# Optimization experiments

Measured on AMD Instinct MI355X. Metric: run time of the kernel, lower is better.

The kernel has to match this reference:

```python
import jax, jax.numpy as jnp
import numpy as np
import math

B, L, D, H, DFF, NL = 32, 512, 768, 12, 3072, 2
E = D // H
VOCAB = 30522
TOPK = int(1 * math.log(L))   # factor=1 -> 6
MA = 25                        # series_decomp moving-average kernel (Autoformer default)
CMID = D // 2                  # 384 conv channels
PLEN = (L - 2) // 2            # 255 pooled length
LATENT, NCELLS = 32, 2034


def _ln(x, g, b, eps=1e-5):
    mu = x.mean(-1, keepdims=True)
    v = ((x - mu) ** 2).mean(-1, keepdims=True)
    return (x - mu) * jax.lax.rsqrt(v + eps) * g + b


def _decomp(x):
    # series_decomp: x - moving_avg(x, k=25) with replicate padding, via cumsum
    pad = (MA - 1) // 2
    xp = jnp.concatenate([jnp.repeat(x[:, :1], pad, 1), x, jnp.repeat(x[:, -1:], pad, 1)], 1)
    cs = jnp.cumsum(xp, axis=1)
    cs = jnp.concatenate([jnp.zeros_like(cs[:, :1]), cs], 1)
    mm = (cs[:, MA:] - cs[:, :-MA]) / MA  # [B,L,D]
    return x - mm


def _autocorr(q, k, v):
    # q,k,v: [B,L,H,E] -> FFT autocorrelation + top-k delay aggregation (inference path)
    qt = jnp.transpose(q, (0, 2, 3, 1))
    kt = jnp.transpose(k, (0, 2, 3, 1))
    vt = jnp.transpose(v, (0, 2, 3, 1))  # [B,H,E,L]
    corr = jnp.fft.irfft(jnp.fft.rfft(qt, axis=-1) * jnp.conj(jnp.fft.rfft(kt, axis=-1)), n=L, axis=-1)
    mean_value = corr.mean(axis=(1, 2))                      # [B,L]
    weights, delay = jax.lax.top_k(mean_value, TOPK)         # [B,K]
    w = jax.nn.softmax(weights, axis=-1)                     # [B,K]
    tv = jnp.concatenate([vt, vt], -1)                       # [B,H,E,2L]
    idx = jnp.arange(L)[None, None, :] + delay[:, :, None]   # [B,K,L]
    pat = jnp.take_along_axis(tv[:, None], idx[:, :, None, None, :], axis=-1)  # [B,K,H,E,L]
    V = jnp.einsum('bkhel,bk->bhel', pat, w)
    return jnp.transpose(V, (0, 3, 1, 2))                    # [B,L,H,E]


def _forward(input_ids, word_emb, pos_emb, tok_emb, emb_ln_g, emb_ln_b,
             Wq, bq, Wk, bk, Wv, bv, Wo, bo, Wc1, bc1, Wc2, bc2,
             norm_g, norm_b, conv_w, conv_b, bn_g, bn_b, bn_m, bn_v,
             lin1_w, lin1_b, ln2_g, ln2_b, lin2_w, lin2_b):
    # BertEmbeddings (token_type all zeros)
    x = word_emb[input_ids] + pos_emb[None, :L] + tok_emb[0][None, None]
    x = _ln(x, emb_ln_g, emb_ln_b, 1e-12)
    # Autoformer encoder layers
    for l in range(NL):
        q = (x @ Wq[l].T + bq[l]).reshape(B, L, H, E)
        k = (x @ Wk[l].T + bk[l]).reshape(B, L, H, E)
        v = (x @ Wv[l].T + bv[l]).reshape(B, L, H, E)
        a = _autocorr(q, k, v).reshape(B, L, D) @ Wo[l].T + bo[l]
        x = _decomp(x + a)
        y = jax.nn.gelu(x @ Wc1[l].T + bc1[l], approximate=False) @ Wc2[l].T + bc2[l]
        x = _decomp(x + y)
    # my_Layernorm
    x_hat = _ln(x, norm_g, norm_b)
    att_out = x_hat - x_hat.mean(axis=1, keepdims=True)      # [B,L,D]
    # Prediction head
    z = jnp.transpose(att_out, (0, 2, 1))                    # [B,D,L]
    c = jax.lax.conv_general_dilated(z, conv_w, (1,), 'VALID',
                                     dimension_numbers=('NCH', 'OIH', 'NCH')) + conv_b[None, :, None]
    c = (c - bn_m[None, :, None]) * jax.lax.rsqrt(bn_v + 1e-5)[None, :, None] * bn_g[None, :, None] + bn_b[None, :, None]
    c = jax.nn.elu(c)                                        # [B,384,510]
    p = c.reshape(B, CMID, PLEN, 2).max(-1)                  # maxpool k=2
    f = p.reshape(B, CMID * PLEN)
    h = jax.nn.elu(_ln(f @ lin1_w.T + lin1_b, ln2_g, ln2_b))
    return jax.nn.sigmoid(h @ lin2_w.T + lin2_b)             # [B,2034]


def setup_inputs() -> dict:
    key = jax.random.key(0)
    ks = iter(jax.random.split(key, 64))
    n = lambda *s: 0.02 * jax.random.normal(next(ks), s, dtype=jnp.float32)
    return dict(
        input_ids=jax.random.randint(next(ks), (B, L), 0, VOCAB),
        word_emb=n(VOCAB, D), pos_emb=n(L, D), tok_emb=n(2, D),
        emb_ln_g=jnp.ones((D,), jnp.float32), emb_ln_b=jnp.zeros((D,), jnp.float32),
        Wq=n(NL, D, D), bq=n(NL, D), Wk=n(NL, D, D), bk=n(NL, D),
        Wv=n(NL, D, D), bv=n(NL, D), Wo=n(NL, D, D), bo=n(NL, D),
        Wc1=n(NL, DFF, D), bc1=n(NL, DFF), Wc2=n(NL, D, DFF), bc2=n(NL, D),
        norm_g=jnp.ones((D,), jnp.float32), norm_b=jnp.zeros((D,), jnp.float32),
        conv_w=n(CMID, D, 3), conv_b=n(CMID),
        bn_g=jnp.ones((CMID,), jnp.float32), bn_b=jnp.zeros((CMID,), jnp.float32),
        bn_m=n(CMID), bn_v=jax.random.uniform(next(ks), (CMID,), jnp.float32) + 0.5,
        lin1_w=n(LATENT, CMID * PLEN), lin1_b=n(LATENT),
        ln2_g=jnp.ones((LATENT,), jnp.float32), ln2_b=jnp.zeros((LATENT,), jnp.float32),
        lin2_w=n(NCELLS, LATENT), lin2_b=n(NCELLS),
    )


def reference(input_ids, word_emb, pos_emb, tok_emb, emb_ln_g, emb_ln_b,
              Wq, bq, Wk, bk, Wv, bv, Wo, bo, Wc1, bc1, Wc2, bc2,
              norm_g, norm_b, conv_w, conv_b, bn_g, bn_b, bn_m, bn_v,
              lin1_w, lin1_b, ln2_g, ln2_b, lin2_w, lin2_b):
    return _forward(input_ids, word_emb, pos_emb, tok_emb, emb_ln_g, emb_ln_b,
                    Wq, bq, Wk, bk, Wv, bv, Wo, bo, Wc1, bc1, Wc2, bc2,
                    norm_g, norm_b, conv_w, conv_b, bn_g, bn_b, bn_m, bn_v,
                    lin1_w, lin1_b, ln2_g, ln2_b, lin2_w, lin2_b)
```

## Files before the change

kernel.cpp:

```cpp
#include <hip/hip_runtime.h>
#include <hip/hip_bf16.h>

#define B_ 32
#define L_ 512
#define D_ 768
#define DFF_ 3072
#define NL_ 2
#define TOPK_ 6
#define CMID_ 384
#define CLEN_ 510
#define PLEN_ 255
#define LATENT_ 32
#define NCELLS_ 2034
#define NROWS_ (B_*L_)
#define ND_ ((size_t)B_*L_*D_)

typedef unsigned short ushort_t;
typedef __attribute__((ext_vector_type(8))) short short8;
typedef __attribute__((ext_vector_type(4))) float f32x4;

typedef const __attribute__((address_space(1))) unsigned int* gp1;
typedef __attribute__((address_space(3))) unsigned int* lp3;

static __device__ __forceinline__ void gload16(const ushort_t* g, ushort_t* l) {
  __builtin_amdgcn_global_load_lds((gp1)g, (lp3)l, 16, 0, 0);
}

static __device__ __forceinline__ float geluf(float x) {
  return 0.5f * x * (1.f + erff(x * 0.70710678118654752440f));
}
static __device__ __forceinline__ float eluf(float x) {
  return x > 0.f ? x : expm1f(x);
}
static __device__ __forceinline__ ushort_t bf16rn(float f) {
  unsigned u = __builtin_bit_cast(unsigned, f);
  u = u + 0x7FFFu + ((u >> 16) & 1u);
  return (ushort_t)(u >> 16);
}
static __device__ __forceinline__ float bf16tof(ushort_t s) {
  unsigned u = ((unsigned)s) << 16;
  return __builtin_bit_cast(float, u);
}
static __device__ __forceinline__ f32x4 mfma16(short8 a, short8 b, f32x4 c) {
  return __builtin_amdgcn_mfma_f32_16x16x32_bf16(a, b, c, 0, 0, 0);
}

__global__ void wsplit(const float* __restrict__ w, ushort_t* __restrict__ hi,
                       ushort_t* __restrict__ lo, size_t n) {
  size_t stride = (size_t)gridDim.x * blockDim.x;
  for (size_t i = (size_t)blockIdx.x * blockDim.x + threadIdx.x; i < n; i += stride) {
    float v = w[i];
    ushort_t h = bf16rn(v);
    hi[i] = h;
    if (lo) lo[i] = bf16rn(v - bf16tof(h));
  }
}

__global__ __launch_bounds__(256) void tsplit(const float* __restrict__ in, ushort_t* __restrict__ hiT,
                                              ushort_t* __restrict__ loT) {
  __shared__ float tile[32][33];
  size_t off = (size_t)blockIdx.z * D_ * D_;
  int bx = blockIdx.x * 32, by = blockIdx.y * 32;
  int tx = threadIdx.x & 31, ty = threadIdx.x >> 5;
#pragma unroll
  for (int i = 0; i < 32; i += 8)
    tile[ty + i][tx] = in[off + (size_t)(by + ty + i) * D_ + bx + tx];
  __syncthreads();
#pragma unroll
  for (int i = 0; i < 32; i += 8) {
    float v = tile[tx][ty + i];
    ushort_t h = bf16rn(v);
    size_t o = off + (size_t)(bx + ty + i) * D_ + by + tx;
    hiT[o] = h;
    loT[o] = bf16rn(v - bf16tof(h));
  }
}

__global__ void bvo_k(const float* __restrict__ wo, const float* __restrict__ bv,
                      const float* __restrict__ bo, float* __restrict__ bvo) {
  int gid = blockIdx.x * 256 + threadIdx.x;
  if (gid >= NL_ * D_) return;
  int l = gid / D_, a = gid % D_;
  const float* w = wo + (size_t)l * D_ * D_ + (size_t)a * D_;
  const float* b = bv + l * D_;
  float s = bo[gid];
  for (int j = 0; j < D_; j++) s = fmaf(w[j], b[j], s);
  bvo[gid] = s;
}

__global__ void conv_w_repack(const float* __restrict__ w, ushort_t* __restrict__ wt) {
  int gid = blockIdx.x * blockDim.x + threadIdx.x;
  if (gid >= CMID_ * 3 * D_) return;
  int o = gid / (3 * D_);
  int k = gid % (3 * D_);
  int j = k / D_, i = k % D_;
  wt[gid] = bf16rn(w[((size_t)o * D_ + i) * 3 + j]);
}

__global__ __launch_bounds__(256) void embed_ln(const int* __restrict__ ids, const float* __restrict__ we,
                                                const float* __restrict__ pe, const float* __restrict__ te,
                                                const float* __restrict__ g, const float* __restrict__ bta,
                                                ushort_t* __restrict__ xh, ushort_t* __restrict__ xl) {
  int row = blockIdx.x;
  int tid = threadIdx.x;
  int t = row & (L_ - 1);
  int id = ids[row];
  float v[3];
#pragma unroll
  for (int dd = 0; dd < 3; dd++) {
    int c = tid + dd * 256;
    v[dd] = we[(size_t)id * D_ + c] + pe[(size_t)t * D_ + c] + te[c];
  }
  float s = v[0] + v[1] + v[2];
  float sq = v[0]*v[0] + v[1]*v[1] + v[2]*v[2];
  __shared__ float rs[256], rq[256];
  rs[tid] = s; rq[tid] = sq;
  __syncthreads();
  for (int st = 128; st > 0; st >>= 1) {
    if (tid < st) { rs[tid] += rs[tid + st]; rq[tid] += rq[tid + st]; }
    __syncthreads();
  }
  __shared__ float smu, ssc;
  if (tid == 0) {
    float mu = rs[0] * (1.f / D_);
    float var = fmaxf(rq[0] * (1.f / D_) - mu * mu, 0.f);
    smu = mu; ssc = rsqrtf(var + 1e-12f);
  }
  __syncthreads();
  float mu = smu, sc = ssc;
#pragma unroll
  for (int dd = 0; dd < 3; dd++) {
    int c = tid + dd * 256;
    size_t o = (size_t)row * D_ + c;
    float ov = (v[dd] - mu) * sc * g[c] + bta[c];
    ushort_t h = bf16rn(ov);
    xh[o] = h;
    xl[o] = bf16rn(ov - bf16tof(h));
  }
}

__global__ __launch_bounds__(256) void ln_pl(const ushort_t* __restrict__ xh, const ushort_t* __restrict__ xl,
                                             float* __restrict__ out,
                                             const float* __restrict__ g, const float* __restrict__ bta,
                                             float eps) {
  int row = blockIdx.x;
  int tid = threadIdx.x;
  size_t base = (size_t)row * D_;
  float v[3];
#pragma unroll
  for (int dd = 0; dd < 3; dd++) {
    size_t o = base + tid + dd * 256;
    v[dd] = bf16tof(xh[o]) + bf16tof(xl[o]);
  }
  float s = v[0] + v[1] + v[2];
  float sq = v[0]*v[0] + v[1]*v[1] + v[2]*v[2];
  __shared__ float rs[256], rq[256];
  rs[tid] = s; rq[tid] = sq;
  __syncthreads();
  for (int st = 128; st > 0; st >>= 1) {
    if (tid < st) { rs[tid] += rs[tid + st]; rq[tid] += rq[tid + st]; }
    __syncthreads();
  }
  __shared__ float smu, ssc;
  if (tid == 0) {
    float mu = rs[0] * (1.f / D_);
    float var = fmaxf(rq[0] * (1.f / D_) - mu * mu, 0.f);
    smu = mu; ssc = rsqrtf(var + eps);
  }
  __syncthreads();
  float mu = smu, sc = ssc;
  float* o = out + base;
#pragma unroll
  for (int dd = 0; dd < 3; dd++) {
    int c = tid + dd * 256;
    o[c] = (v[dd] - mu) * sc * g[c] + bta[c];
  }
}

template<int ACT, bool SPLIT, int EPI>
__global__ __launch_bounds__(256) void gemm_bf16(
    const ushort_t* __restrict__ Ah, const ushort_t* __restrict__ Al,
    const ushort_t* __restrict__ Wh, const ushort_t* __restrict__ Wl,
    const float* __restrict__ bias,
    const ushort_t* __restrict__ ResH, const ushort_t* __restrict__ ResL,
    void* __restrict__ C0, void* __restrict__ C1,
    const float* __restrict__ bn_m, const float* __restrict__ bn_v,
    const float* __restrict__ bn_g, const float* __restrict__ bn_b,
    int O, int K, int lda,
    long long sA, long long sW, long long sC,
    int nbx, int nby) {
  constexpr int NP = SPLIT ? 2 : 1;
  __shared__ __align__(16) ushort_t AsH[NP][128 * 64];
  __shared__ __align__(16) ushort_t WsH[NP][128 * 64];
  __shared__ float dsum[EPI == 3 ? 512 : 1];

  int nwg = gridDim.x;
  int wg = blockIdx.x;
  {
    int qq = nwg >> 3, rr = nwg & 7;
    int xcd = wg & 7, idx = wg >> 3;
    wg = (xcd < rr ? xcd * (qq + 1) : rr * (qq + 1) + (xcd - rr) * qq) + idx;
  }
  int per_b = nbx * nby;
  int bz = wg / per_b;
  int rem = wg - bz * per_b;
  int gsz = nbx * 8;
  int grp = rem / gsz;
  int ing = rem - grp * gsz;
  int by0 = grp * 8;
  int gmx = min(8, nby - by0);
  int by = by0 + (ing % gmx);
  int bx = ing / gmx;

  const ushort_t* Ahb = Ah + (size_t)bz * sA;
  const ushort_t* Alb = SPLIT ? (Al + (size_t)bz * sA) : nullptr;
  const ushort_t* Whb = Wh + (size_t)bz * sW;
  const ushort_t* Wlb = SPLIT ? (Wl + (size_t)bz * sW) : nullptr;

  int m0 = by * 128, o0 = bx * 128;
  int tid = threadIdx.x;
  int wave = tid >> 6, lane = tid & 63;
  int wm = (wave >> 1) * 64, wn = (wave & 1) * 64;
  int lcol = lane & 15, lk = lane >> 4;

  if (EPI == 3) {
    for (int s = tid; s < 512; s += 256) dsum[s] = 0.f;
  }

  f32x4 acc[4][4] = {};

  int r8 = lane >> 3;
  int kc = (((lane & 7) ^ r8) << 3);

  const ushort_t *gA[4], *gW[4], *gAl[4], *gWl[4];
#pragma unroll
  for (int i = 0; i < 4; i++) {
    int ch = wave * 4 + i;
    int row = ch * 8 + r8;
    size_t oa = (size_t)(m0 + row) * lda + kc;
    size_t ow = (size_t)(o0 + row) * K + kc;
    gA[i] = Ahb + oa; gW[i] = Whb + ow;
    if (SPLIT) { gAl[i] = Alb + oa; gWl[i] = Wlb + ow; }
  }

  for (int k0 = 0; k0 < K; k0 += 64) {
#pragma unroll
    for (int i = 0; i < 4; i++) {
      int ch = wave * 4 + i;
      gload16(gA[i], &AsH[0][ch * 512]); gA[i] += 64;
      gload16(gW[i], &WsH[0][ch * 512]); gW[i] += 64;
      if (SPLIT) {
        gload16(gAl[i], &AsH[1][ch * 512]); gAl[i] += 64;
        gload16(gWl[i], &WsH[1][ch * 512]); gWl[i] += 64;
      }
    }
    __syncthreads();
#pragma unroll
    for (int kk = 0; kk < 2; kk++) {
      int c = kk * 4 + lk;
      short8 ah[4], bh[4], al[4], bl[4];
#pragma unroll
      for (int i = 0; i < 4; i++) {
        int r = wm + i * 16 + lcol;
        int so = r * 64 + ((c ^ (r & 7)) << 3);
        ah[i] = *(const short8*)&AsH[0][so];
        if (SPLIT) al[i] = *(const short8*)&AsH[1][so];
      }
#pragma unroll
      for (int j = 0; j < 4; j++) {
        int r = wn + j * 16 + lcol;
        int so = r * 64 + ((c ^ (r & 7)) << 3);
        bh[j] = *(const short8*)&WsH[0][so];
        if (SPLIT) bl[j] = *(const short8*)&WsH[1][so];
      }
#pragma unroll
      for (int i = 0; i < 4; i++)
#pragma unroll
        for (int j = 0; j < 4; j++) {
          if (SPLIT) {
            acc[i][j] = mfma16(ah[i], bl[j], acc[i][j]);
            acc[i][j] = mfma16(al[i], bh[j], acc[i][j]);
          }
          acc[i][j] = mfma16(ah[i], bh[j], acc[i][j]);
        }
    }
    __syncthreads();
  }

  if (EPI == 3) {
    float pre[7][4] = {};
#pragma unroll
    for (int i = 0; i < 4; i++)
#pragma unroll
      for (int j = 0; j < 4; j++)
#pragma unroll
        for (int r = 0; r < 4; r++)
          pre[i - j + 3][r] += acc[i][j][r];
    int base = (m0 + wm + lk * 4) - (o0 + wn + lcol);
#pragma unroll
    for (int g = 0; g < 7; g++)
#pragma unroll
      for (int r = 0; r < 4; r++)
        atomicAdd(&dsum[(base + 16 * (g - 3) + r) & (L_ - 1)], pre[g][r]);
    __syncthreads();
    float* mvp = (float*)C0;
    int blk = by * nbx + bx;
    for (int s = tid; s < 512; s += 256)
      mvp[((size_t)bz * 16 + blk) * 512 + s] = dsum[s] * (1.f / D_);
  } else if (EPI == 4) {
#pragma unroll
    for (int j = 0; j < 4; j++) {
      int col = o0 + wn + j * 16 + lcol;
      float cbias = bias[col];
      float sc = rsqrtf(bn_v[col] + 1e-5f) * bn_g[col];
      float shf = bn_b[col] - bn_m[col] * sc;
#pragma unroll
      for (int i = 0; i < 4; i++) {
        int rowb = m0 + wm + i * 16 + lk * 4;
        int t = rowb & (L_ - 1);
        int b = rowb >> 9;
#pragma unroll
        for (int p = 0; p < 2; p++) {
          int tt = t + p * 2;
          if (tt >= CLEN_) continue;
          float v0 = eluf((acc[i][j][p * 2]     + cbias) * sc + shf);
          float v1 = eluf((acc[i][j][p * 2 + 1] + cbias) * sc + shf);
          ((float*)C0)[((size_t)b * CMID_ + col) * PLEN_ + (tt >> 1)] = fmaxf(v0, v1);
        }
      }
    }
  } else {
#pragma unroll
    for (int i = 0; i < 4; i++)
#pragma unroll
      for (int j = 0; j < 4; j++) {
        int col = o0 + wn + j * 16 + lcol;
        float bv = bias ? bias[col] : 0.f;
        int rowb = m0 + wm + i * 16 + lk * 4;
#pragma unroll
        for (int r = 0; r < 4; r++) {
          float v = acc[i][j][r] + bv;
          if (ACT == 1) v = geluf(v);
          size_t off = (size_t)bz * sC + (size_t)(rowb + r) * O + col;
          if (EPI == 0) {
            if (ResH) v += bf16tof(ResH[off]) + bf16tof(ResL[off]);
            ((float*)C0)[off] = v;
          }
          if (EPI == 1) ((ushort_t*)C0)[off] = bf16rn(v);
          if (EPI == 2) {
            ushort_t h = bf16rn(v);
            ((ushort_t*)C0)[off] = h;
            ((ushort_t*)C1)[off] = bf16rn(v - bf16tof(h));
          }
        }
      }
  }
}

__global__ __launch_bounds__(256) void topk_softmax(const float* __restrict__ mvp,
                                                    float* __restrict__ wout, int* __restrict__ dout) {
  int b = blockIdx.x, tid = threadIdx.x;
  __shared__ float vals[L_];
  __shared__ float rv[256];
  __shared__ int ri[256];
  __shared__ float wsel[TOPK_];
  __shared__ int dsel[TOPK_];
  float s0 = 0.f, s1 = 0.f;
  for (int p = 0; p < 16; p++) {
    const float* pp = mvp + ((size_t)b * 16 + p) * L_;
    s0 += pp[tid]; s1 += pp[tid + 256];
  }
  vals[tid] = s0; vals[tid + 256] = s1;
  for (int kk = 0; kk < TOPK_; kk++) {
    __syncthreads();
    float v0 = vals[tid], v1 = vals[tid + 256];
    float bvv = v0; int bi = tid;
    if (v1 > v0) { bvv = v1; bi = tid + 256; }
    rv[tid] = bvv; ri[tid] = bi;
    __syncthreads();
    for (int st = 128; st > 0; st >>= 1) {
      if (tid < st) {
        float ov = rv[tid + st]; int oi = ri[tid + st];
        if (ov > rv[tid] || (ov == rv[tid] && oi < ri[tid])) { rv[tid] = ov; ri[tid] = oi; }
      }
      __syncthreads();
    }
    if (tid == 0) { wsel[kk] = rv[0]; dsel[kk] = ri[0]; vals[ri[0]] = -INFINITY; }
  }
  __syncthreads();
  if (tid == 0) {
    float mx = wsel[0];
    for (int i = 1; i < TOPK_; i++) mx = fmaxf(mx, wsel[i]);
    float e[TOPK_]; float sum = 0.f;
    for (int i = 0; i < TOPK_; i++) { e[i] = expf(wsel[i] - mx); sum += e[i]; }
    for (int i = 0; i < TOPK_; i++) { wout[b * TOPK_ + i] = e[i] / sum; dout[b * TOPK_ + i] = dsel[i]; }
  }
}

__global__ __launch_bounds__(256) void agg_res(const ushort_t* __restrict__ P, const float* __restrict__ w,
                                               const int* __restrict__ dly,
                                               const ushort_t* __restrict__ xh, const ushort_t* __restrict__ xl,
                                               float* __restrict__ y) {
  int blr = blockIdx.x;
  int b = blr >> 9, t = blr & 511;
  int tid = threadIdx.x;
  __shared__ float ww[TOPK_];
  __shared__ int rr[TOPK_];
  if (tid < TOPK_) { ww[tid] = w[b * TOPK_ + tid]; rr[tid] = (t + dly[b * TOPK_ + tid]) & (L_ - 1); }
  __syncthreads();
  const ushort_t* pb = P + (size_t)b * L_ * D_;
#pragma unroll
  for (int dd = 0; dd < 3; dd++) {
    int d = tid + dd * 256;
    size_t o = (size_t)blr * D_ + d;
    float s = bf16tof(xh[o]) + bf16tof(xl[o]);
#pragma unroll
    for (int kk = 0; kk < TOPK_; kk++)
      s = fmaf(ww[kk], bf16tof(pb[(size_t)rr[kk] * D_ + d]), s);
    y[o] = s;
  }
}

__global__ void decomp_pl(const float* __restrict__ s,
                          ushort_t* __restrict__ xh, ushort_t* __restrict__ xl) {
  int gid = blockIdx.x * blockDim.x + threadIdx.x;
  if (gid >= B_ * 8 * D_) return;
  int d = gid % D_;
  int chunk = (gid / D_) & 7;
  int b = gid / (D_ * 8);
  size_t base = (size_t)b * L_ * D_ + d;
  int t0 = chunk * 64;
  float wsum = 0.f;
  for (int u = t0 - 12; u <= t0 + 12; u++) {
    int uc = u < 0 ? 0 : (u > L_ - 1 ? L_ - 1 : u);
    wsum += s[base + (size_t)uc * D_];
  }
  for (int t = t0; t < t0 + 64; t++) {
    size_t o = base + (size_t)t * D_;
    float v = s[o] - wsum * (1.f / 25.f);
    ushort_t h = bf16rn(v);
    xh[o] = h;
    xl[o] = bf16rn(v - bf16tof(h));
    int ua = t + 13 > L_ - 1 ? L_ - 1 : t + 13;
    int ur = t - 12 < 0 ? 0 : t - 12;
    wsum += s[base + (size_t)ua * D_] - s[base + (size_t)ur * D_];
  }
}

__global__ void colmean_bf16(const float* __restrict__ x, ushort_t* __restrict__ sh) {
  int gid = blockIdx.x * blockDim.x + threadIdx.x;
  if (gid >= B_ * D_) return;
  int d = gid % D_, b = gid / D_;
  const float* col = x + (size_t)b * L_ * D_ + d;
  ushort_t* oc = sh + (size_t)b * L_ * D_ + d;
  float s = 0.f;
  for (int t = 0; t < L_; t++) s += col[(size_t)t * D_];
  float mu = s * (1.f / L_);
  for (int t = 0; t < L_; t++) oc[(size_t)t * D_] = bf16rn(col[(size_t)t * D_] - mu);
}

__global__ __launch_bounds__(256) void lin1_k(const float* __restrict__ f, const float* __restrict__ w,
                                              const float* __restrict__ bias, float* __restrict__ out) {
  int o = blockIdx.x, b = blockIdx.y;
  int tid = threadIdx.x;
  const float4* fr = (const float4*)(f + (size_t)b * (CMID_ * PLEN_));
  const float4* wr = (const float4*)(w + (size_t)o * (CMID_ * PLEN_));
  const int n4 = CMID_ * PLEN_ / 4;
  float s = 0.f;
  for (int i = tid; i < n4; i += 256) {
    float4 a = fr[i], ww = wr[i];
    s += a.x * ww.x + a.y * ww.y + a.z * ww.z + a.w * ww.w;
  }
  __shared__ float red[256];
  red[tid] = s;
  __syncthreads();
  for (int st = 128; st > 0; st >>= 1) {
    if (tid < st) red[tid] += red[tid + st];
    __syncthreads();
  }
  if (tid == 0) out[b * LATENT_ + o] = red[0] + bias[o];
}

__global__ void ln_elu(const float* __restrict__ hp, const float* __restrict__ g,
                       const float* __restrict__ bb, float* __restrict__ h) {
  int b = blockIdx.x;
  int tid = threadIdx.x;
  __shared__ float v[LATENT_];
  __shared__ float mu_s, sc_s;
  if (tid < LATENT_) v[tid] = hp[b * LATENT_ + tid];
  __syncthreads();
  if (tid == 0) {
    float s = 0.f, sq = 0.f;
    for (int i = 0; i < LATENT_; i++) { s += v[i]; sq += v[i] * v[i]; }
    float mu = s * (1.f / LATENT_);
    float var = fmaxf(sq * (1.f / LATENT_) - mu * mu, 0.f);
    mu_s = mu; sc_s = rsqrtf(var + 1e-5f);
  }
  __syncthreads();
  if (tid < LATENT_) h[b * LATENT_ + tid] = eluf((v[tid] - mu_s) * sc_s * g[tid] + bb[tid]);
}

__global__ void lin2_sig(const float* __restrict__ h, const float* __restrict__ w,
                         const float* __restrict__ bias, float* __restrict__ out) {
  int gid = blockIdx.x * blockDim.x + threadIdx.x;
  if (gid >= B_ * NCELLS_) return;
  int b = gid / NCELLS_, c = gid % NCELLS_;
  const float* hr = h + b * LATENT_;
  const float* wr = w + (size_t)c * LATENT_;
  float s = bias[c];
  for (int j = 0; j < LATENT_; j++) s = fmaf(hr[j], wr[j], s);
  out[gid] = 1.f / (1.f + expf(-s));
}

extern "C" void kernel_launch(void* const* d_in, const int* in_sizes, int n_in,
                              void* d_out, int out_size, void* d_ws, size_t ws_size,
                              hipStream_t stream) {
  const int*   ids  = (const int*)  d_in[0];
  const float* we   = (const float*)d_in[1];
  const float* pe   = (const float*)d_in[2];
  const float* te   = (const float*)d_in[3];
  const float* elng = (const float*)d_in[4];
  const float* elnb = (const float*)d_in[5];
  const float* Wq   = (const float*)d_in[6];
  const float* bq   = (const float*)d_in[7];   (void)bq;
  const float* Wk   = (const float*)d_in[8];
  const float* bk   = (const float*)d_in[9];   (void)bk;
  const float* Wv   = (const float*)d_in[10];
  const float* bv   = (const float*)d_in[11];
  const float* Wo   = (const float*)d_in[12];
  const float* bo   = (const float*)d_in[13];
  const float* Wc1  = (const float*)d_in[14];
  const float* bc1  = (const float*)d_in[15];
  const float* Wc2  = (const float*)d_in[16];
  const float* bc2  = (const float*)d_in[17];
  const float* ng   = (const float*)d_in[18];
  const float* nb   = (const float*)d_in[19];
  const float* cw   = (const float*)d_in[20];
  const float* cb   = (const float*)d_in[21];
  const float* bng  = (const float*)d_in[22];
  const float* bnb  = (const float*)d_in[23];
  const float* bnm  = (const float*)d_in[24];
  const float* bnv  = (const float*)d_in[25];
  const float* l1w  = (const float*)d_in[26];
  const float* l1b  = (const float*)d_in[27];
  const float* l2g  = (const float*)d_in[28];
  const float* l2b  = (const float*)d_in[29];
  const float* l2w  = (const float*)d_in[30];
  const float* l2bi = (const float*)d_in[31];
  float* out = (float*)d_out;

  char* wp = (char*)d_ws;
  auto alloc = [&](size_t bytes) { char* p = wp; wp += (bytes + 255) & ~(size_t)255; return p; };
  ushort_t* Xh  = (ushort_t*)alloc(ND_ * 2);
  ushort_t* Xl  = (ushort_t*)alloc(ND_ * 2);
  ushort_t* R1  = (ushort_t*)alloc(ND_ * 2 * 4);
  char*     PvB = (char*)    alloc(ND_ * 4);
  float*    Y   = (float*)   alloc(ND_ * 4);
  float*    MVP = (float*)   alloc((size_t)B_ * 16 * L_ * 4);
  float*    WT  = (float*)   alloc(B_ * TOPK_ * 4);
  int*      DT  = (int*)     alloc(B_ * TOPK_ * 4);
  float*    HP  = (float*)   alloc(B_ * LATENT_ * 4);
  float*    HH  = (float*)   alloc(B_ * LATENT_ * 4);
  const size_t DD = (size_t)D_ * D_, DF = (size_t)DFF_ * D_;
  ushort_t* MTh  = (ushort_t*)alloc(NL_ * DD * 2);
  ushort_t* MTl  = (ushort_t*)alloc(NL_ * DD * 2);
  ushort_t* WvoH = (ushort_t*)alloc(NL_ * DD * 2);
  float*    BVO  = (float*)   alloc(NL_ * D_ * 4);
  ushort_t* W1H  = (ushort_t*)alloc(NL_ * DF * 2);
  ushort_t* W2H  = (ushort_t*)alloc(NL_ * DF * 2);
  ushort_t* WTC  = (ushort_t*)alloc((size_t)CMID_ * 3 * D_ * 2);

  ushort_t* XMh = R1;
  ushort_t* XMl = R1 + ND_;
  ushort_t* Gh  = R1;
  float*    F   = (float*)R1;
  ushort_t* Pb  = (ushort_t*)PvB;
  float*    LNo = (float*)PvB;
  ushort_t* Sh  = Xh;

  ushort_t* SC = R1;
  ushort_t* WqTh = SC;                ushort_t* WqTl = SC + 1 * NL_ * DD;
  ushort_t* WkTh = SC + 2 * NL_ * DD; ushort_t* WkTl = SC + 3 * NL_ * DD;
  ushort_t* WvTh = SC + 4 * NL_ * DD; ushort_t* WvTl = SC + 5 * NL_ * DD;
  ushort_t* WoH  = SC + 6 * NL_ * DD; ushort_t* WoL  = SC + 7 * NL_ * DD;

  tsplit<<<dim3(24, 24, NL_), 256, 0, stream>>>(Wq, WqTh, WqTl);
  tsplit<<<dim3(24, 24, NL_), 256, 0, stream>>>(Wk, WkTh, WkTl);
  tsplit<<<dim3(24, 24, NL_), 256, 0, stream>>>(Wv, WvTh, WvTl);
  wsplit<<<512, 256, 0, stream>>>(Wo, WoH, WoL, NL_ * DD);
  wsplit<<<1024, 256, 0, stream>>>(Wc1, W1H, nullptr, NL_ * DF);
  wsplit<<<1024, 256, 0, stream>>>(Wc2, W2H, nullptr, NL_ * DF);
  conv_w_repack<<<(CMID_ * 3 * D_ + 255) / 256, 256, 0, stream>>>(cw, WTC);

  gemm_bf16<0, true, 2><<<72, 256, 0, stream>>>(WkTh, WkTl, WqTh, WqTl, nullptr, nullptr, nullptr,
                                                MTh, MTl, nullptr, nullptr, nullptr, nullptr,
                                                D_, D_, D_, (long long)DD, (long long)DD, (long long)DD, 6, 6);
  gemm_bf16<0, true, 1><<<72, 256, 0, stream>>>(WoH, WoL, WvTh, WvTl, nullptr, nullptr, nullptr,
                                                WvoH, nullptr, nullptr, nullptr, nullptr, nullptr,
                                                D_, D_, D_, (long long)DD, (long long)DD, (long long)DD, 6, 6);
  bvo_k<<<(NL_ * D_ + 255) / 256, 256, 0, stream>>>(Wo, bv, bo, BVO);

  embed_ln<<<NROWS_, 256, 0, stream>>>(ids, we, pe, te, elng, elnb, Xh, Xl);

  for (int l = 0; l < NL_; l++) {
    gemm_bf16<0, true, 2><<<768, 256, 0, stream>>>(Xh, Xl, MTh + l*DD, MTl + l*DD, nullptr, nullptr, nullptr,
                                                   XMh, XMl, nullptr, nullptr, nullptr, nullptr,
                                                   D_, D_, D_, 0, 0, 0, 6, 128);
    gemm_bf16<0, false, 1><<<768, 256, 0, stream>>>(Xh, nullptr, WvoH + l*DD, nullptr, BVO + l*D_, nullptr, nullptr,
                                                    Pb, nullptr, nullptr, nullptr, nullptr, nullptr,
                                                    D_, D_, D_, 0, 0, 0, 6, 128);
    gemm_bf16<0, true, 3><<<512, 256, 0, stream>>>(XMh, XMl, Xh, Xl, nullptr, nullptr, nullptr,
                                                   MVP, nullptr, nullptr, nullptr, nullptr, nullptr,
                                                   L_, D_, D_, (long long)L_ * D_, (long long)L_ * D_, 0, 4, 4);
    topk_softmax<<<B_, 256, 0, stream>>>(MVP, WT, DT);
    agg_res<<<NROWS_, 256, 0, stream>>>(Pb, WT, DT, Xh, Xl, Y);
    decomp_pl<<<(B_ * 8 * D_) / 256, 256, 0, stream>>>(Y, Xh, Xl);
    gemm_bf16<1, false, 1><<<3072, 256, 0, stream>>>(Xh, nullptr, W1H + l*DF, nullptr, bc1 + l*DFF_, nullptr, nullptr,
                                                     Gh, nullptr, nullptr, nullptr, nullptr, nullptr,
                                                     DFF_, D_, D_, 0, 0, 0, 24, 128);
    gemm_bf16<0, false, 0><<<768, 256, 0, stream>>>(Gh, nullptr, W2H + l*DF, nullptr, bc2 + l*D_, Xh, Xl,
                                                    Y, nullptr, nullptr, nullptr, nullptr, nullptr,
                                                    D_, DFF_, DFF_, 0, 0, 0, 6, 128);
    decomp_pl<<<(B_ * 8 * D_) / 256, 256, 0, stream>>>(Y, Xh, Xl);
  }

  ln_pl<<<NROWS_, 256, 0, stream>>>(Xh, Xl, LNo, ng, nb, 1e-5f);
  colmean_bf16<<<(B_ * D_ + 255) / 256, 256, 0, stream>>>(LNo, Sh);

  gemm_bf16<0, false, 4><<<384, 256, 0, stream>>>(Sh, nullptr, WTC, nullptr, cb, nullptr, nullptr,
                                                  F, nullptr, bnm, bnv, bng, bnb,
                                                  CMID_, 3 * D_, D_, 0, 0, 0, 3, 128);
  lin1_k<<<dim3(LATENT_, B_), 256, 0, stream>>>(F, l1w, l1b, HP);
  ln_elu<<<B_, 64, 0, stream>>>(HP, l2g, l2b, HH);
  lin2_sig<<<(B_ * NCELLS_ + 255) / 256, 256, 0, stream>>>(HH, l2w, l2bi, out);
}
```

Measured before the change: 1.244 ms.

## Add 256x256-tile 8-wave pipelined GEMM for FFN and value projections

```diff
diff --git a/kernel.cpp b/kernel.cpp
--- a/kernel.cpp
+++ b/kernel.cpp
@@ -174,6 +174,123 @@
   for (int dd = 0; dd < 3; dd++) {
     int c = tid + dd * 256;
     o[c] = (v[dd] - mu) * sc * g[c] + bta[c];
+  }
+}
+
+template<int ACT, int EPI>
+__global__ __launch_bounds__(512, 1) void gemm8p(
+    const ushort_t* __restrict__ A, const ushort_t* __restrict__ W,
+    const float* __restrict__ bias,
+    const ushort_t* __restrict__ ResH, const ushort_t* __restrict__ ResL,
+    void* __restrict__ C0, int O, int K, int lda, int nbx, int nby) {
+  __shared__ __align__(16) ushort_t Asm[2][16384];
+  __shared__ __align__(16) ushort_t Bsm[2][16384];
+
+  int nwg = gridDim.x;
+  int wg = blockIdx.x;
+  {
+    int qq = nwg >> 3, rr = nwg & 7;
+    int xcd = wg & 7, idx = wg >> 3;
+    wg = (xcd < rr ? xcd * (qq + 1) : rr * (qq + 1) + (xcd - rr) * qq) + idx;
+  }
+  int gsz = nbx * 8;
+  int grp = wg / gsz;
+  int ing = wg - grp * gsz;
+  int by0 = grp * 8;
+  int gmx = min(8, nby - by0);
+  int by = by0 + (ing % gmx);
+  int bx = ing / gmx;
+
+  int m0 = by * 256, o0 = bx * 256;
+  int tid = threadIdx.x;
+  int wave = tid >> 6, lane = tid & 63;
+  int wm = wave >> 2, wn = wave & 3;
+  int lcol = lane & 15, lk = lane >> 4;
+  int swzl = (lcol & 3) ^ ((lcol >> 2) & 3);
+  int sloA = ((lk ^ swzl) << 3);
+  int srcsw = (((tid & 3) ^ ((tid >> 2) & 3) ^ ((tid >> 4) & 3)) << 3);
+  int nt = K >> 6;
+  int niter = nt >> 1;
+
+  f32x4 acc[8][4] = {};
+
+  auto STAGE = [&](int T, int mat, int kh) {
+    if (T >= nt) return;
+    ushort_t* lb = (mat == 0 ? &Asm[T & 1][kh * 8192 + (wave << 9)]
+                             : &Bsm[T & 1][kh * 8192 + (wave << 9)]);
+    const ushort_t* gb = (mat == 0 ? A : W);
+    int ld = (mat == 0 ? lda : K);
+    int br = (mat == 0 ? m0 : o0) + (tid >> 2);
+    int cc = T * 64 + kh * 32 + srcsw;
+    gload16(gb + (size_t)br * ld + cc, lb);
+    gload16(gb + (size_t)(br + 128) * ld + cc, lb + 4096);
+  };
+
+#define PHASE_(bufi, mh, kh, sT, sM, sK)                                         \
+  {                                                                              \
+    short8 af[4], bfr[4];                                                        \
+    _Pragma("unroll")                                                            \
+    for (int fi = 0; fi < 4; fi++)                                               \
+      af[fi] = *(const short8*)&Asm[bufi][(kh) * 8192 +                          \
+               (wm * 128 + (mh) * 64 + fi * 16 + lcol) * 32 + sloA];             \
+    _Pragma("unroll")                                                            \
+    for (int fj = 0; fj < 4; fj++)                                               \
+      bfr[fj] = *(const short8*)&Bsm[bufi][(kh) * 8192 +                         \
+               (wn * 64 + fj * 16 + lcol) * 32 + sloA];                          \
+    STAGE(sT, sM, sK);                                                           \
+    __builtin_amdgcn_s_barrier();                                                \
+    asm volatile("s_waitcnt lgkmcnt(0)" ::: "memory");                           \
+    __builtin_amdgcn_sched_barrier(0);                                           \
+    __builtin_amdgcn_s_setprio(1);                                               \
+    _Pragma("unroll")                                                            \
+    for (int fi = 0; fi < 4; fi++)                                               \
+      _Pragma("unroll")                                                          \
+      for (int fj = 0; fj < 4; fj++)                                             \
+        acc[(mh) * 4 + fi][fj] = mfma16(af[fi], bfr[fj], acc[(mh) * 4 + fi][fj]);\
+    __builtin_amdgcn_s_setprio(0);                                               \
+    __builtin_amdgcn_s_barrier();                                                \
+  }
+
+  STAGE(0, 0, 0); STAGE(0, 1, 0); STAGE(0, 0, 1); STAGE(0, 1, 1);
+  STAGE(1, 0, 0); STAGE(1, 1, 0);
+
+  for (int i = 0; i < niter; i++) {
+    int E = 2 * i;
+    asm volatile("s_waitcnt vmcnt(4)" ::: "memory");
+    __builtin_amdgcn_s_barrier();
+    PHASE_(0, 0, 0, E + 1, 0, 1);
+    PHASE_(0, 1, 0, E + 1, 1, 1);
+    PHASE_(0, 0, 1, E + 2, 0, 0);
+    PHASE_(0, 1, 1, E + 2, 1, 0);
+    if (i + 1 == niter) asm volatile("s_waitcnt vmcnt(0)" ::: "memory");
+    else                asm volatile("s_waitcnt vmcnt(4)" ::: "memory");
+    __builtin_amdgcn_s_barrier();
+    PHASE_(1, 0, 0, E + 2, 0, 1);
+    PHASE_(1, 1, 0, E + 2, 1, 1);
+    PHASE_(1, 0, 1, E + 3, 0, 0);
+    PHASE_(1, 1, 1, E + 3, 1, 0);
+  }
+#undef PHASE_
+
+#pragma unroll
+  for (int fi = 0; fi < 8; fi++) {
+    int rowb = m0 + wm * 128 + fi * 16 + lk * 4;
+#pragma unroll
+    for (int fj = 0; fj < 4; fj++) {
+      int col = o0 + wn * 64 + fj * 16 + lcol;
+      float bv = bias ? bias[col] : 0.f;
+#pragma unroll
+      for (int r = 0; r < 4; r++) {
+        float v = acc[fi][fj][r] + bv;
+        if (ACT == 1) v = geluf(v);
+        size_t off = (size_t)(rowb + r) * O + col;
+        if (EPI == 0) {
+          if (ResH) v += bf16tof(ResH[off]) + bf16tof(ResL[off]);
+          ((float*)C0)[off] = v;
+        }
+        if (EPI == 1) ((ushort_t*)C0)[off] = bf16rn(v);
+      }
+    }
   }
 }
 
@@ -606,21 +723,18 @@
     gemm_bf16<0, true, 2><<<768, 256, 0, stream>>>(Xh, Xl, MTh + l*DD, MTl + l*DD, nullptr, nullptr, nullptr,
                                                    XMh, XMl, nullptr, nullptr, nullptr, nullptr,
                                                    D_, D_, D_, 0, 0, 0, 6, 128);
-    gemm_bf16<0, false, 1><<<768, 256, 0, stream>>>(Xh, nullptr, WvoH + l*DD, nullptr, BVO + l*D_, nullptr, nullptr,
-                                                    Pb, nullptr, nullptr, nullptr, nullptr, nullptr,
-                                                    D_, D_, D_, 0, 0, 0, 6, 128);
+    gemm8p<0, 1><<<192, 512, 0, stream>>>(Xh, WvoH + l*DD, BVO + l*D_, nullptr, nullptr,
+                                          Pb, D_, D_, D_, 3, 64);
     gemm_bf16<0, true, 3><<<512, 256, 0, stream>>>(XMh, XMl, Xh, Xl, nullptr, nullptr, nullptr,
                                                    MVP, nullptr, nullptr, nullptr, nullptr, nullptr,
                                                    L_, D_, D_, (long long)L_ * D_, (long long)L_ * D_, 0, 4, 4);
     topk_softmax<<<B_, 256, 0, stream>>>(MVP, WT, DT);
     agg_res<<<NROWS_, 256, 0, stream>>>(Pb, WT, DT, Xh, Xl, Y);
     decomp_pl<<<(B_ * 8 * D_) / 256, 256, 0, stream>>>(Y, Xh, Xl);
-    gemm_bf16<1, false, 1><<<3072, 256, 0, stream>>>(Xh, nullptr, W1H + l*DF, nullptr, bc1 + l*DFF_, nullptr, nullptr,
-                                                     Gh, nullptr, nullptr, nullptr, nullptr, nullptr,
-                                                     DFF_, D_, D_, 0, 0, 0, 24, 128);
-    gemm_bf16<0, false, 0><<<768, 256, 0, stream>>>(Gh, nullptr, W2H + l*DF, nullptr, bc2 + l*D_, Xh, Xl,
-                                                    Y, nullptr, nullptr, nullptr, nullptr, nullptr,
-                                                    D_, DFF_, DFF_, 0, 0, 0, 6, 128);
+    gemm8p<1, 1><<<768, 512, 0, stream>>>(Xh, W1H + l*DF, bc1 + l*DFF_, nullptr, nullptr,
+                                          Gh, DFF_, D_, D_, 12, 64);
+    gemm8p<0, 0><<<192, 512, 0, stream>>>(Gh, W2H + l*DF, bc2 + l*D_, Xh, Xl,
+                                          Y, D_, DFF_, DFF_, 3, 64);
     decomp_pl<<<(B_ * 8 * D_) / 256, 256, 0, stream>>>(Y, Xh, Xl);
   }
 
```

After: 1.371 ms. 10.2% more time.

## Fuse autocorrelation aggregation with series decomposition and batch weight-prep kernels

Applied to the files above, without the earlier changes.

```diff
diff --git a/kernel.cpp b/kernel.cpp
--- a/kernel.cpp
+++ b/kernel.cpp
@@ -56,10 +56,18 @@
   }
 }
 
-__global__ __launch_bounds__(256) void tsplit(const float* __restrict__ in, ushort_t* __restrict__ hiT,
-                                              ushort_t* __restrict__ loT) {
+__global__ __launch_bounds__(256) void tsplit3(const float* __restrict__ w0, const float* __restrict__ w1,
+                                               const float* __restrict__ w2,
+                                               ushort_t* __restrict__ h0, ushort_t* __restrict__ l0p,
+                                               ushort_t* __restrict__ h1, ushort_t* __restrict__ l1p,
+                                               ushort_t* __restrict__ h2, ushort_t* __restrict__ l2p) {
   __shared__ float tile[32][33];
-  size_t off = (size_t)blockIdx.z * D_ * D_;
+  int z = blockIdx.z;
+  int m = z / NL_, l = z % NL_;
+  const float* in = (m == 0) ? w0 : (m == 1 ? w1 : w2);
+  ushort_t* hiT = (m == 0) ? h0 : (m == 1 ? h1 : h2);
+  ushort_t* loT = (m == 0) ? l0p : (m == 1 ? l1p : l2p);
+  size_t off = (size_t)l * D_ * D_;
   int bx = blockIdx.x * 32, by = blockIdx.y * 32;
   int tx = threadIdx.x & 31, ty = threadIdx.x >> 5;
 #pragma unroll
@@ -397,27 +405,38 @@
   }
 }
 
-__global__ __launch_bounds__(256) void agg_res(const ushort_t* __restrict__ P, const float* __restrict__ w,
-                                               const int* __restrict__ dly,
-                                               const ushort_t* __restrict__ xh, const ushort_t* __restrict__ xl,
-                                               float* __restrict__ y) {
-  int blr = blockIdx.x;
-  int b = blr >> 9, t = blr & 511;
-  int tid = threadIdx.x;
-  __shared__ float ww[TOPK_];
-  __shared__ int rr[TOPK_];
-  if (tid < TOPK_) { ww[tid] = w[b * TOPK_ + tid]; rr[tid] = (t + dly[b * TOPK_ + tid]) & (L_ - 1); }
-  __syncthreads();
-  const ushort_t* pb = P + (size_t)b * L_ * D_;
-#pragma unroll
-  for (int dd = 0; dd < 3; dd++) {
-    int d = tid + dd * 256;
-    size_t o = (size_t)blr * D_ + d;
+__global__ void agg_decomp(const ushort_t* __restrict__ P, const float* __restrict__ w,
+                           const int* __restrict__ dly,
+                           const ushort_t* __restrict__ xh, const ushort_t* __restrict__ xl,
+                           ushort_t* __restrict__ oh, ushort_t* __restrict__ ol) {
+  int gid = blockIdx.x * blockDim.x + threadIdx.x;
+  if (gid >= B_ * 8 * D_) return;
+  int d = gid % D_;
+  int chunk = (gid / D_) & 7;
+  int b = gid / (D_ * 8);
+  size_t base = (size_t)b * L_ * D_ + d;
+  float ww[TOPK_]; int dk[TOPK_];
+#pragma unroll
+  for (int k = 0; k < TOPK_; k++) { ww[k] = w[b * TOPK_ + k]; dk[k] = dly[b * TOPK_ + k]; }
+  auto Yat = [&](int t) -> float {
+    int tc = t < 0 ? 0 : (t > L_ - 1 ? L_ - 1 : t);
+    size_t o = base + (size_t)tc * D_;
     float s = bf16tof(xh[o]) + bf16tof(xl[o]);
 #pragma unroll
-    for (int kk = 0; kk < TOPK_; kk++)
-      s = fmaf(ww[kk], bf16tof(pb[(size_t)rr[kk] * D_ + d]), s);
-    y[o] = s;
+    for (int k = 0; k < TOPK_; k++)
+      s = fmaf(ww[k], bf16tof(P[base + (size_t)((tc + dk[k]) & (L_ - 1)) * D_]), s);
+    return s;
+  };
+  int t0 = chunk * 64;
+  float wsum = 0.f;
+  for (int u = t0 - 12; u <= t0 + 12; u++) wsum += Yat(u);
+  for (int t = t0; t < t0 + 64; t++) {
+    float v = Yat(t) - wsum * (1.f / 25.f);
+    size_t o = base + (size_t)t * D_;
+    ushort_t h = bf16rn(v);
+    oh[o] = h;
+    ol[o] = bf16rn(v - bf16tof(h));
+    wsum += Yat(t + 13) - Yat(t - 12);
   }
 }
 
@@ -553,6 +572,8 @@
   auto alloc = [&](size_t bytes) { char* p = wp; wp += (bytes + 255) & ~(size_t)255; return p; };
   ushort_t* Xh  = (ushort_t*)alloc(ND_ * 2);
   ushort_t* Xl  = (ushort_t*)alloc(ND_ * 2);
+  ushort_t* X2h = (ushort_t*)alloc(ND_ * 2);
+  ushort_t* X2l = (ushort_t*)alloc(ND_ * 2);
   ushort_t* R1  = (ushort_t*)alloc(ND_ * 2 * 4);
   char*     PvB = (char*)    alloc(ND_ * 4);
   float*    Y   = (float*)   alloc(ND_ * 4);
@@ -562,13 +583,16 @@
   float*    HP  = (float*)   alloc(B_ * LATENT_ * 4);
   float*    HH  = (float*)   alloc(B_ * LATENT_ * 4);
   const size_t DD = (size_t)D_ * D_, DF = (size_t)DFF_ * D_;
-  ushort_t* MTh  = (ushort_t*)alloc(NL_ * DD * 2);
-  ushort_t* MTl  = (ushort_t*)alloc(NL_ * DD * 2);
-  ushort_t* WvoH = (ushort_t*)alloc(NL_ * DD * 2);
+  ushort_t* PCC_h = (ushort_t*)alloc(4 * DD * 2);
+  ushort_t* PCC_l = (ushort_t*)alloc(4 * DD * 2);
   float*    BVO  = (float*)   alloc(NL_ * D_ * 4);
   ushort_t* W1H  = (ushort_t*)alloc(NL_ * DF * 2);
   ushort_t* W2H  = (ushort_t*)alloc(NL_ * DF * 2);
   ushort_t* WTC  = (ushort_t*)alloc((size_t)CMID_ * 3 * D_ * 2);
+
+  ushort_t* MTh  = PCC_h;
+  ushort_t* MTl  = PCC_l;
+  ushort_t* WvoH = PCC_h + NL_ * DD;
 
   ushort_t* XMh = R1;
   ushort_t* XMl = R1 + ND_;
@@ -576,28 +600,28 @@
   float*    F   = (float*)R1;
   ushort_t* Pb  = (ushort_t*)PvB;
   float*    LNo = (float*)PvB;
-  ushort_t* Sh  = Xh;
+  ushort_t* Sh  = X2h;
 
   ushort_t* SC = R1;
-  ushort_t* WqTh = SC;                ushort_t* WqTl = SC + 1 * NL_ * DD;
-  ushort_t* WkTh = SC + 2 * NL_ * DD; ushort_t* WkTl = SC + 3 * NL_ * DD;
-  ushort_t* WvTh = SC + 4 * NL_ * DD; ushort_t* WvTl = SC + 5 * NL_ * DD;
-  ushort_t* WoH  = SC + 6 * NL_ * DD; ushort_t* WoL  = SC + 7 * NL_ * DD;
-
-  tsplit<<<dim3(24, 24, NL_), 256, 0, stream>>>(Wq, WqTh, WqTl);
-  tsplit<<<dim3(24, 24, NL_), 256, 0, stream>>>(Wk, WkTh, WkTl);
-  tsplit<<<dim3(24, 24, NL_), 256, 0, stream>>>(Wv, WvTh, WvTl);
+  ushort_t* PCA_h = SC;
+  ushort_t* PCA_l = SC + 4 * DD;
+  ushort_t* PCW_h = SC + 8 * DD;
+  ushort_t* PCW_l = SC + 12 * DD;
+  ushort_t* WkTh = PCA_h;                 ushort_t* WkTl = PCA_l;
+  ushort_t* WoH  = PCA_h + NL_ * DD;      ushort_t* WoL  = PCA_l + NL_ * DD;
+  ushort_t* WqTh = PCW_h;                 ushort_t* WqTl = PCW_l;
+  ushort_t* WvTh = PCW_h + NL_ * DD;      ushort_t* WvTl = PCW_l + NL_ * DD;
+
+  tsplit3<<<dim3(24, 24, 3 * NL_), 256, 0, stream>>>(Wq, Wk, Wv,
+                                                     WqTh, WqTl, WkTh, WkTl, WvTh, WvTl);
   wsplit<<<512, 256, 0, stream>>>(Wo, WoH, WoL, NL_ * DD);
   wsplit<<<1024, 256, 0, stream>>>(Wc1, W1H, nullptr, NL_ * DF);
   wsplit<<<1024, 256, 0, stream>>>(Wc2, W2H, nullptr, NL_ * DF);
   conv_w_repack<<<(CMID_ * 3 * D_ + 255) / 256, 256, 0, stream>>>(cw, WTC);
 
-  gemm_bf16<0, true, 2><<<72, 256, 0, stream>>>(WkTh, WkTl, WqTh, WqTl, nullptr, nullptr, nullptr,
-                                                MTh, MTl, nullptr, nullptr, nullptr, nullptr,
-                                                D_, D_, D_, (long long)DD, (long long)DD, (long long)DD, 6, 6);
-  gemm_bf16<0, true, 1><<<72, 256, 0, stream>>>(WoH, WoL, WvTh, WvTl, nullptr, nullptr, nullptr,
-                                                WvoH, nullptr, nullptr, nullptr, nullptr, nullptr,
-                                                D_, D_, D_, (long long)DD, (long long)DD, (long long)DD, 6, 6);
+  gemm_bf16<0, true, 2><<<144, 256, 0, stream>>>(PCA_h, PCA_l, PCW_h, PCW_l, nullptr, nullptr, nullptr,
+                                                 PCC_h, PCC_l, nullptr, nullptr, nullptr, nullptr,
+                                                 D_, D_, D_, (long long)DD, (long long)DD, (long long)DD, 6, 6);
   bvo_k<<<(NL_ * D_ + 255) / 256, 256, 0, stream>>>(Wo, bv, bo, BVO);
 
   embed_ln<<<NROWS_, 256, 0, stream>>>(ids, we, pe, te, elng, elnb, Xh, Xl);
@@ -613,12 +637,11 @@
                                                    MVP, nullptr, nullptr, nullptr, nullptr, nullptr,
                                                    L_, D_, D_, (long long)L_ * D_, (long long)L_ * D_, 0, 4, 4);
     topk_softmax<<<B_, 256, 0, stream>>>(MVP, WT, DT);
-    agg_res<<<NROWS_, 256, 0, stream>>>(Pb, WT, DT, Xh, Xl, Y);
-    decomp_pl<<<(B_ * 8 * D_) / 256, 256, 0, stream>>>(Y, Xh, Xl);
-    gemm_bf16<1, false, 1><<<3072, 256, 0, stream>>>(Xh, nullptr, W1H + l*DF, nullptr, bc1 + l*DFF_, nullptr, nullptr,
+    agg_decomp<<<(B_ * 8 * D_) / 256, 256, 0, stream>>>(Pb, WT, DT, Xh, Xl, X2h, X2l);
+    gemm_bf16<1, false, 1><<<3072, 256, 0, stream>>>(X2h, nullptr, W1H + l*DF, nullptr, bc1 + l*DFF_, nullptr, nullptr,
                                                      Gh, nullptr, nullptr, nullptr, nullptr, nullptr,
                                                      DFF_, D_, D_, 0, 0, 0, 24, 128);
-    gemm_bf16<0, false, 0><<<768, 256, 0, stream>>>(Gh, nullptr, W2H + l*DF, nullptr, bc2 + l*D_, Xh, Xl,
+    gemm_bf16<0, false, 0><<<768, 256, 0, stream>>>(Gh, nullptr, W2H + l*DF, nullptr, bc2 + l*D_, X2h, X2l,
                                                     Y, nullptr, nullptr, nullptr, nullptr, nullptr,
                                                     D_, DFF_, DFF_, 0, 0, 0, 6, 128);
     decomp_pl<<<(B_ * 8 * D_) / 256, 256, 0, stream>>>(Y, Xh, Xl);
```

Result: slower. 1.347 ms (+8.3%).
